# Kernel tuning notes

Hardware: AMD Instinct MI355X
Metric: run time of the kernel (lower is better)

Reference implementation:

```python
import jax, jax.numpy as jnp
import numpy as np

GROUPS = 32
K = 5          # up_kernel_size
UP = 2         # up_factor
EPS = 1e-5


def group_norm(x, w, b):
    B, C, H, W = x.shape
    xr = x.reshape(B, GROUPS, -1)
    mu = xr.mean(axis=2, keepdims=True)
    var = xr.var(axis=2, keepdims=True)
    xr = (xr - mu) * jax.lax.rsqrt(var + EPS)
    return xr.reshape(B, C, H, W) * w[None, :, None, None] + b[None, :, None, None]


def setup_inputs() -> dict:
    key = jax.random.key(0)
    ks = jax.random.split(key, 4)
    B, Cy, Cx, E, H, W = 4, 256, 256, 32, 64, 64
    return {
        "y": jax.random.normal(ks[0], (B, Cy, H * UP, W * UP), jnp.float32),
        "x": jax.random.normal(ks[1], (B, Cx, H, W), jnp.float32),
        "gn_y_w": jnp.ones((Cy,), jnp.float32),
        "gn_y_b": jnp.zeros((Cy,), jnp.float32),
        "gn_x_w": jnp.ones((Cx,), jnp.float32),
        "gn_x_b": jnp.zeros((Cx,), jnp.float32),
        "q_w": jax.random.normal(ks[2], (E, Cy), jnp.float32) * 0.02,
        "q_b": jnp.zeros((E,), jnp.float32),
        "k_w": jax.random.normal(ks[3], (E, Cx), jnp.float32) * 0.02,
        "k_b": jnp.zeros((E,), jnp.float32),
    }


def reference(y, x, gn_y_w, gn_y_b, gn_x_w, gn_x_b, q_w, q_b, k_w, k_b):
    pad = K // 2
    yn = group_norm(y, gn_y_w, gn_y_b)
    xn = group_norm(x, gn_x_w, gn_x_b)
    # 1x1 convs
    q = jnp.einsum('bchw,ec->behw', yn, q_w) + q_b[None, :, None, None]  # [B,E,Hu,Wu]
    k = jnp.einsum('bchw,ec->behw', xn, k_w) + k_b[None, :, None, None]  # [B,E,H,W]
    B, E, H, W = k.shape
    C = x.shape[1]
    # view q as per-low-res-cell blocks of UPxUP high-res queries
    q_r = q.reshape(B, E, H, UP, W, UP)
    k_pad = jnp.pad(k, ((0, 0), (0, 0), (pad, pad), (pad, pad)))  # zero pad (out-of-range -> 0 logit)
    v_pad = jnp.pad(x, ((0, 0), (0, 0), (pad, pad), (pad, pad)))
    # qk: logits over the KxK window (loop over 25 fixed offsets, vectorized inside)
    logits = []
    for dy in range(K):
        for dx in range(K):
            ks = k_pad[:, :, dy:dy + H, dx:dx + W]            # [B,E,H,W]
            logits.append(jnp.einsum('behuwv,behw->bhuwv', q_r, ks))
    logits = jnp.stack(logits, axis=1)                        # [B,KK,H,u,W,u]
    attn = jax.nn.softmax(logits, axis=1)
    # av: weighted aggregation of v over the same window
    out = jnp.zeros((B, C, H, UP, W, UP), x.dtype)
    idx = 0
    for dy in range(K):
        for dx in range(K):
            vs = v_pad[:, :, dy:dy + H, dx:dx + W]            # [B,C,H,W]
            out = out + attn[:, idx][:, None] * vs[:, :, :, None, :, None]
            idx += 1
    return out.reshape(B, C, H * UP, W * UP)
```

## Files before the change

kernel.cpp:

```cpp
#include <hip/hip_runtime.h>

#define EPSV 1e-5f

__global__ __launch_bounds__(256) void stats_kernel(const float* __restrict__ y,
                                                    const float* __restrict__ x,
                                                    float* __restrict__ part) {
    int bid = blockIdx.x;
    const float* src = (bid < 1024) ? (y + (size_t)bid * 16384)
                                    : (x + (size_t)(bid - 1024) * 16384);
    const float4* p = (const float4*)src;
    float s = 0.f, ss = 0.f;
    #pragma unroll 8
    for (int i = threadIdx.x; i < 4096; i += 256) {
        float4 v = p[i];
        s  += v.x + v.y + v.z + v.w;
        ss += v.x*v.x + v.y*v.y + v.z*v.z + v.w*v.w;
    }
    for (int off = 32; off > 0; off >>= 1) {
        s  += __shfl_down(s, off);
        ss += __shfl_down(ss, off);
    }
    __shared__ float red[8];
    int wid = threadIdx.x >> 6, lane = threadIdx.x & 63;
    if (lane == 0) { red[wid*2] = s; red[wid*2+1] = ss; }
    __syncthreads();
    if (threadIdx.x == 0) {
        part[bid*2+0] = red[0] + red[2] + red[4] + red[6];
        part[bid*2+1] = red[1] + red[3] + red[5] + red[7];
    }
}

__global__ __launch_bounds__(64) void make_eff_kernel(const float* __restrict__ qw, const float* __restrict__ qb,
                                                      const float* __restrict__ gyw, const float* __restrict__ gyb,
                                                      const float* __restrict__ kw, const float* __restrict__ kb,
                                                      const float* __restrict__ gxw, const float* __restrict__ gxb,
                                                      const float* __restrict__ part,
                                                      float* __restrict__ WeffQ, float* __restrict__ beffQ,
                                                      float* __restrict__ WeffK, float* __restrict__ beffK) {
    int id = blockIdx.x;
    int isK = id >> 7, b = (id >> 5) & 3, e = id & 31;
    const float* w     = isK ? kw  : qw;
    const float* bias  = isK ? kb  : qb;
    const float* gamma = isK ? gxw : gyw;
    const float* beta  = isK ? gxb : gyb;
    float inv_n = isK ? (1.f/32768.f) : (1.f/131072.f);
    float* W  = isK ? WeffK : WeffQ;
    float* be = isK ? beffK : beffQ;
    float partial = 0.f;
    for (int c = threadIdx.x; c < 256; c += 64) {
        int g = c >> 3, grp = b*32 + g;
        float s = 0.f, ss = 0.f;
        if (isK) {
            #pragma unroll
            for (int k2 = 0; k2 < 2; ++k2) {
                s  += part[(1024 + grp*2 + k2)*2 + 0];
                ss += part[(1024 + grp*2 + k2)*2 + 1];
            }
        } else {
            #pragma unroll
            for (int k2 = 0; k2 < 8; ++k2) {
                s  += part[(grp*8 + k2)*2 + 0];
                ss += part[(grp*8 + k2)*2 + 1];
            }
        }
        float mu = s * inv_n;
        float rs = rsqrtf(fmaf(-mu, mu, ss * inv_n) + EPSV);
        float wc = w[e*256 + c];
        float weff = wc * gamma[c] * rs;
        W[((size_t)b*256 + c)*32 + e] = weff;
        partial += wc * beta[c] - weff * mu;
    }
    for (int off = 32; off > 0; off >>= 1) partial += __shfl_down(partial, off);
    if (threadIdx.x == 0) be[b*32 + e] = partial + bias[e];
}

__global__ __launch_bounds__(64) void proj_kernel(const float* __restrict__ y, const float* __restrict__ x,
                                                  const float* __restrict__ WeffQ, const float* __restrict__ beffQ,
                                                  const float* __restrict__ WeffK, const float* __restrict__ beffK,
                                                  float* __restrict__ qbuf, float* __restrict__ kbuf) {
    int bid = blockIdx.x;
    int isX = bid >= 1024;
    int lb  = isX ? bid - 1024 : bid;
    int b   = isX ? (lb >> 6) : (lb >> 8);
    int pxb = isX ? (lb & 63) : (lb & 255);
    int npix = isX ? 4096 : 16384;
    const float* src   = isX ? x : y;
    const float* WeffT = isX ? WeffK : WeffQ;
    const float* beff  = isX ? beffK : beffQ;
    float* dst = isX ? kbuf : qbuf;

    int pix = pxb * 64 + threadIdx.x;
    float acc[32];
    #pragma unroll
    for (int j = 0; j < 32; ++j) acc[j] = beff[b*32 + j];

    const float* sp    = src + (size_t)b*256*npix + pix;
    const float* wbase = WeffT + (size_t)b*256*32;
    #pragma unroll 4
    for (int c = 0; c < 256; ++c) {
        float t = sp[(size_t)c*npix];
        const float* wc = wbase + c*32;
        #pragma unroll
        for (int j = 0; j < 32; ++j) acc[j] = fmaf(t, wc[j], acc[j]);
    }

    float* dbase = dst + ((size_t)b*npix + pix)*32;
    #pragma unroll
    for (int j4 = 0; j4 < 8; ++j4) {
        float4 o = {acc[j4*4+0], acc[j4*4+1], acc[j4*4+2], acc[j4*4+3]};
        *(float4*)(dbase + j4*4) = o;
    }
}

__global__ __launch_bounds__(512) void attn_weights_kernel(const float* __restrict__ q,
                                                           const float* __restrict__ kk,
                                                           float* __restrict__ g_attn)
{
    __shared__ __align__(16) float sK[5184];
    int h0 = blockIdx.y * 8, w0 = blockIdx.x * 8;
    int b = blockIdx.z;
    int tid = threadIdx.x;

    for (int i = tid; i < 1152; i += 512) {
        int pos = i >> 3, e4 = i & 7;
        int r = pos / 12, c = pos - 12*r;
        int gh = h0 + r - 2, gw = w0 + c - 2;
        float4 v = make_float4(0.f, 0.f, 0.f, 0.f);
        if (gh >= 0 && gh < 64 && gw >= 0 && gw < 64)
            v = *(const float4*)(kk + (((size_t)b*4096 + gh*64 + gw)*32 + e4*4));
        *(float4*)&sK[pos*36 + e4*4] = v;
    }

    int wave = tid >> 6;
    int lane = tid & 63;
    int eq   = lane >> 5;
    int cl   = lane & 31;
    int child = wave*32 + cl;
    int h = wave;
    int u = (cl >> 4) & 1, w = (cl >> 1) & 7, v = cl & 1;

    float qv[16];
    {
        int hh = 2*(h0 + h) + u, ww = 2*(w0 + w) + v;
        const float4* qp = (const float4*)(q + (((size_t)b*16384 + hh*128 + ww)*32 + eq*16));
        #pragma unroll
        for (int i4 = 0; i4 < 4; ++i4) {
            float4 t = qp[i4];
            qv[i4*4+0]=t.x; qv[i4*4+1]=t.y; qv[i4*4+2]=t.z; qv[i4*4+3]=t.w;
        }
    }
    __syncthreads();

    float a[25];
    const float* kbase = &sK[(h*12 + w)*36 + eq*16];
    #pragma unroll
    for (int j = 0; j < 25; ++j) {
        int dy = j / 5, dx = j - 5*dy;
        const float4* kp = (const float4*)(kbase + (dy*12 + dx)*36);
        float acc = 0.f;
        #pragma unroll
        for (int e4 = 0; e4 < 4; ++e4) {
            float4 kv = kp[e4];
            acc = fmaf(qv[e4*4+0], kv.x, acc);
            acc = fmaf(qv[e4*4+1], kv.y, acc);
            acc = fmaf(qv[e4*4+2], kv.z, acc);
            acc = fmaf(qv[e4*4+3], kv.w, acc);
        }
        a[j] = acc;
    }
    #pragma unroll
    for (int j = 0; j < 25; ++j) a[j] += __shfl_xor(a[j], 32);

    float m = -1e30f;
    #pragma unroll
    for (int j = 0; j < 25; ++j) m = fmaxf(m, a[j]);
    float s = 0.f;
    #pragma unroll
    for (int j = 0; j < 25; ++j) { a[j] = __expf(a[j] - m); s += a[j]; }
    float inv = 1.f / s;

    float* gbase = g_attn + ((size_t)b*64 + blockIdx.y*8 + blockIdx.x)*6400 + child;
    if (eq == 0) {
        #pragma unroll
        for (int jj = 0; jj < 13; ++jj) gbase[(2*jj)*256] = a[2*jj] * inv;
    } else {
        #pragma unroll
        for (int jj = 0; jj < 12; ++jj) gbase[(2*jj+1)*256] = a[2*jj+1] * inv;
    }
}

__global__ __launch_bounds__(256) void gather_kernel(const float* __restrict__ g_attn,
                                                     const float* __restrict__ x,
                                                     float* __restrict__ out)
{
    __shared__ __align__(16) float sX[2880];
    int h0 = blockIdx.y * 8, w0 = blockIdx.x * 8;
    int b = blockIdx.z >> 4, chunk = blockIdx.z & 15;
    int tid = threadIdx.x;

    float a[25];
    {
        const float* abase = g_attn + ((size_t)b*64 + blockIdx.y*8 + blockIdx.x)*6400 + tid;
        #pragma unroll
        for (int j = 0; j < 25; ++j) a[j] = abase[j*256];
    }

    for (int i = 0; i < 9; ++i) {
        int t = i*256 + tid;
        int cc = t / 144, pos = t - 144*cc;
        int r = pos / 12, cl = pos - 12*r;
        int gh = h0 + r - 2, gw = w0 + cl - 2;
        float val = 0.f;
        if (gh >= 0 && gh < 64 && gw >= 0 && gw < 64)
            val = x[(((size_t)b*256 + chunk*16 + cc)*64 + gh)*64 + gw];
        sX[pos*20 + cc] = val;
    }

    int h = tid >> 5, u = (tid >> 4) & 1, w = (tid >> 1) & 7, v = tid & 1;
    int hh = 2*(h0 + h) + u, ww = 2*(w0 + w) + v;
    int vbase = (h*12 + w)*20;
    __syncthreads();

    #pragma unroll
    for (int g = 0; g < 4; ++g) {
        float o0 = 0.f, o1 = 0.f, o2 = 0.f, o3 = 0.f;
        const float* xb = &sX[vbase + g*4];
        #pragma unroll
        for (int j = 0; j < 25; ++j) {
            int dy = j / 5, dx = j - 5*dy;
            float4 xv = *(const float4*)(xb + (dy*12 + dx)*20);
            float aw = a[j];
            o0 = fmaf(aw, xv.x, o0);
            o1 = fmaf(aw, xv.y, o1);
            o2 = fmaf(aw, xv.z, o2);
            o3 = fmaf(aw, xv.w, o3);
        }
        size_t ob = (((size_t)b*256 + chunk*16 + g*4)*128 + hh)*128 + ww;
        out[ob]           = o0;
        out[ob + 16384]   = o1;
        out[ob + 32768]   = o2;
        out[ob + 49152]   = o3;
    }
}

extern "C" void kernel_launch(void* const* d_in, const int* in_sizes, int n_in,
                              void* d_out, int out_size, void* d_ws, size_t ws_size,
                              hipStream_t stream) {
    const float* y   = (const float*)d_in[0];
    const float* x   = (const float*)d_in[1];
    const float* gyw = (const float*)d_in[2];
    const float* gyb = (const float*)d_in[3];
    const float* gxw = (const float*)d_in[4];
    const float* gxb = (const float*)d_in[5];
    const float* qw  = (const float*)d_in[6];
    const float* qb  = (const float*)d_in[7];
    const float* kw  = (const float*)d_in[8];
    const float* kb  = (const float*)d_in[9];
    float* out = (float*)d_out;
    float* ws  = (float*)d_ws;

    float* part   = ws;
    float* WeffQ  = ws + 2560;
    float* beffQ  = ws + 35328;
    float* WeffK  = ws + 35456;
    float* beffK  = ws + 68224;
    float* qbuf   = ws + 68352;
    float* kbuf   = ws + 2165504;
    float* attnbf = ws + 2689792;

    stats_kernel<<<1280, 256, 0, stream>>>(y, x, part);
    make_eff_kernel<<<256, 64, 0, stream>>>(qw, qb, gyw, gyb, kw, kb, gxw, gxb,
                                            part, WeffQ, beffQ, WeffK, beffK);
    proj_kernel<<<1280, 64, 0, stream>>>(y, x, WeffQ, beffQ, WeffK, beffK, qbuf, kbuf);
    attn_weights_kernel<<<dim3(8, 8, 4), 512, 0, stream>>>(qbuf, kbuf, attnbf);
    gather_kernel<<<dim3(8, 8, 64), 256, 0, stream>>>(attnbf, x, out);
}
```

Baseline: 221.1 us.

## Stage proj_kernel input through double-buffered LDS and split output channels across waves

The 1x1 projection kernel now runs 128 threads per block. Each wave computes half of the 32 output channels for 64 pixels, and the input channel rows are staged in 32-channel chunks through a double-buffered shared-memory tile using float4 global loads. The next chunk is prefetched into registers while the current chunk is computed. This is meant to cut per-thread accumulator pressure, raise occupancy, and hide global load latency. In exchange it adds two block barriers per chunk and extra LDS traffic.

```diff
diff --git a/kernel.cpp b/kernel.cpp
--- a/kernel.cpp
+++ b/kernel.cpp
@@ -74,10 +74,11 @@
     if (threadIdx.x == 0) be[b*32 + e] = partial + bias[e];
 }
 
-__global__ __launch_bounds__(64) void proj_kernel(const float* __restrict__ y, const float* __restrict__ x,
-                                                  const float* __restrict__ WeffQ, const float* __restrict__ beffQ,
-                                                  const float* __restrict__ WeffK, const float* __restrict__ beffK,
-                                                  float* __restrict__ qbuf, float* __restrict__ kbuf) {
+__global__ __launch_bounds__(128) void proj_kernel(const float* __restrict__ y, const float* __restrict__ x,
+                                                   const float* __restrict__ WeffQ, const float* __restrict__ beffQ,
+                                                   const float* __restrict__ WeffK, const float* __restrict__ beffK,
+                                                   float* __restrict__ qbuf, float* __restrict__ kbuf) {
+    __shared__ __align__(16) float sY[2][2048];
     int bid = blockIdx.x;
     int isX = bid >= 1024;
     int lb  = isX ? bid - 1024 : bid;
@@ -89,24 +90,61 @@
     const float* beff  = isX ? beffK : beffQ;
     float* dst = isX ? kbuf : qbuf;
 
-    int pix = pxb * 64 + threadIdx.x;
-    float acc[32];
-    #pragma unroll
-    for (int j = 0; j < 32; ++j) acc[j] = beff[b*32 + j];
-
-    const float* sp    = src + (size_t)b*256*npix + pix;
-    const float* wbase = WeffT + (size_t)b*256*32;
-    #pragma unroll 4
-    for (int c = 0; c < 256; ++c) {
-        float t = sp[(size_t)c*npix];
-        const float* wc = wbase + c*32;
-        #pragma unroll
-        for (int j = 0; j < 32; ++j) acc[j] = fmaf(t, wc[j], acc[j]);
-    }
-
-    float* dbase = dst + ((size_t)b*npix + pix)*32;
-    #pragma unroll
-    for (int j4 = 0; j4 < 8; ++j4) {
+    int tid = threadIdx.x;
+    int px  = tid & 63;
+    int eg  = __builtin_amdgcn_readfirstlane(tid >> 6);
+    int px0 = pxb * 64;
+
+    const float* srcb = src + (size_t)b*256*npix + px0;
+    int srow = tid >> 4;
+    int scol = (tid & 15) * 4;
+
+    float acc[16];
+    #pragma unroll
+    for (int j = 0; j < 16; ++j) acc[j] = beff[b*32 + eg*16 + j];
+
+    #pragma unroll
+    for (int k = 0; k < 4; ++k) {
+        float4 t = *(const float4*)(srcb + (size_t)(srow + k*8)*npix + scol);
+        *(float4*)&sY[0][(srow + k*8)*64 + scol] = t;
+    }
+    __syncthreads();
+
+    const float* wb = WeffT + (size_t)b*8192 + eg*16;
+    #pragma unroll 1
+    for (int ch = 0; ch < 8; ++ch) {
+        int cur = ch & 1;
+        float4 r0, r1, r2, r3;
+        if (ch < 7) {
+            int c0n = (ch + 1) * 32;
+            r0 = *(const float4*)(srcb + (size_t)(c0n + srow     )*npix + scol);
+            r1 = *(const float4*)(srcb + (size_t)(c0n + srow + 8 )*npix + scol);
+            r2 = *(const float4*)(srcb + (size_t)(c0n + srow + 16)*npix + scol);
+            r3 = *(const float4*)(srcb + (size_t)(c0n + srow + 24)*npix + scol);
+        }
+        const float* sb = &sY[cur][px];
+        int c0 = ch * 32;
+        #pragma unroll
+        for (int cc = 0; cc < 32; ++cc) {
+            float t = sb[cc*64];
+            const float* wr = wb + (c0 + cc)*32;
+            #pragma unroll
+            for (int j = 0; j < 16; ++j) acc[j] = fmaf(t, wr[j], acc[j]);
+        }
+        if (ch < 7) {
+            __syncthreads();
+            int nb = cur ^ 1;
+            *(float4*)&sY[nb][(srow     )*64 + scol] = r0;
+            *(float4*)&sY[nb][(srow + 8 )*64 + scol] = r1;
+            *(float4*)&sY[nb][(srow + 16)*64 + scol] = r2;
+            *(float4*)&sY[nb][(srow + 24)*64 + scol] = r3;
+            __syncthreads();
+        }
+    }
+
+    float* dbase = dst + ((size_t)b*npix + px0 + px)*32 + eg*16;
+    #pragma unroll
+    for (int j4 = 0; j4 < 4; ++j4) {
         float4 o = {acc[j4*4+0], acc[j4*4+1], acc[j4*4+2], acc[j4*4+3]};
         *(float4*)(dbase + j4*4) = o;
     }
@@ -271,7 +309,7 @@
     stats_kernel<<<1280, 256, 0, stream>>>(y, x, part);
     make_eff_kernel<<<256, 64, 0, stream>>>(qw, qb, gyw, gyb, kw, kb, gxw, gxb,
                                             part, WeffQ, beffQ, WeffK, beffK);
-    proj_kernel<<<1280, 64, 0, stream>>>(y, x, WeffQ, beffQ, WeffK, beffK, qbuf, kbuf);
+    proj_kernel<<<1280, 128, 0, stream>>>(y, x, WeffQ, beffQ, WeffK, beffK, qbuf, kbuf);
     attn_weights_kernel<<<dim3(8, 8, 4), 512, 0, stream>>>(qbuf, kbuf, attnbf);
     gather_kernel<<<dim3(8, 8, 64), 256, 0, stream>>>(attnbf, x, out);
 }
```

Result: slower. 265.0 us (+19.8%).
